# Performance work log

Hardware: AMD Instinct MI355X
Metric: run time of the kernel (lower is better)

The kernel has to match this reference:

```python
import jax, jax.numpy as jnp
import numpy as np

NUM_SEGMENTS = 64  # number of bags
L, D, F = 1024, 256, 32  # D = L/4, F = D/8, K = 1
EPS = 1e-12  # torch F.normalize eps


def setup_inputs() -> dict:
    key = jax.random.key(0)
    ks = jax.random.split(key, 10)
    N = 262144
    x = jax.random.normal(ks[0], (N, L), dtype=jnp.float32)
    idxs = jnp.sort(jax.random.randint(ks[1], (N,), 0, NUM_SEGMENTS)).astype(jnp.int64)
    sc = lambda fan_in: 1.0 / np.sqrt(fan_in)
    W1 = jax.random.uniform(ks[2], (L, D), jnp.float32, -sc(L), sc(L))
    b1 = jax.random.uniform(ks[3], (D,), jnp.float32, -sc(L), sc(L))
    Wa1 = jax.random.uniform(ks[4], (D, F), jnp.float32, -sc(D), sc(D))
    ba1 = jax.random.uniform(ks[5], (F,), jnp.float32, -sc(D), sc(D))
    Wa2 = jax.random.uniform(ks[6], (F, 1), jnp.float32, -sc(F), sc(F))
    ba2 = jax.random.uniform(ks[7], (1,), jnp.float32, -sc(F), sc(F))
    Wp = jax.random.uniform(ks[8], (D, F), jnp.float32, -sc(D), sc(D))
    bp = jax.random.uniform(ks[9], (F,), jnp.float32, -sc(D), sc(D))
    return {"x": x, "idxs": idxs, "W1": W1, "b1": b1, "Wa1": Wa1, "ba1": ba1,
            "Wa2": Wa2, "ba2": ba2, "Wp": Wp, "bp": bp}


def reference(x, idxs, W1, b1, Wa1, ba1, Wa2, ba2, Wp, bp):
    seg = idxs.astype(jnp.int32)
    # feature extractor (Dropout is identity in eval): H [N, D]
    H = x @ W1 + b1
    # attention logits: tanh MLP -> [N]
    logits = (jnp.tanh(H @ Wa1 + ba1) @ Wa2 + ba2)[:, 0]
    # segment softmax over instances within each bag
    m = jax.ops.segment_max(logits, seg, num_segments=NUM_SEGMENTS)
    e = jnp.exp(logits - m[seg])
    s = jax.ops.segment_sum(e, seg, num_segments=NUM_SEGMENTS)
    w = e / s[seg]  # [N]
    # attention-weighted bag embeddings: M [B, D]
    M = jax.ops.segment_sum(w[:, None] * H, seg, num_segments=NUM_SEGMENTS)
    # projector + L2 normalize (torch F.normalize: x / max(||x||, eps))
    proj = M @ Wp + bp
    norm = jnp.linalg.norm(proj, axis=1, keepdims=True)
    proj = proj / jnp.maximum(norm, EPS)
    return (M, proj)
```

## Files before the change

kernel.cpp:

```cpp
#include <hip/hip_runtime.h>
#include <stdint.h>

#define LDIM 1024
#define DDIM 256
#define FDIM 32
#define NSEG 64
#define BM 128
#define BK 64

typedef __attribute__((ext_vector_type(4))) float f32x4;
typedef __attribute__((ext_vector_type(8))) short short8;
typedef __attribute__((ext_vector_type(4))) unsigned int u32x4;

__device__ __forceinline__ unsigned int pk2bf(float a, float b) {
  union { float f; unsigned int u; } x, y; x.f = a; y.f = b;
  unsigned int ua = x.u + 0x7FFFu + ((x.u >> 16) & 1u);
  unsigned int ub = y.u + 0x7FFFu + ((y.u >> 16) & 1u);
  return (ua >> 16) | (ub & 0xFFFF0000u);
}

__device__ __forceinline__ unsigned short f2bf(float f) {
  union { float f; unsigned int u; } v; v.f = f;
  unsigned int r = v.u + 0x7FFFu + ((v.u >> 16) & 1u);
  return (unsigned short)(r >> 16);
}

__global__ void prep_w1t(const float* __restrict__ W1, const float* __restrict__ Wa1,
                         unsigned short* __restrict__ w1t) {
  __shared__ float rowf[DDIM];
  const int k = blockIdx.x;
  const int t = threadIdx.x;
  float v = W1[(size_t)k * DDIM + t];
  rowf[t] = v;
  w1t[(size_t)t * LDIM + k] = f2bf(v);
  __syncthreads();
  if (t < FDIM) {
    float a = 0.f;
    for (int c = 0; c < DDIM; ++c) a += rowf[c] * Wa1[c * FDIM + t];
    w1t[(size_t)(DDIM + t) * LDIM + k] = f2bf(a);
  }
}

__global__ void prep_misc(const float* __restrict__ b1, const float* __restrict__ Wa1,
                          const float* __restrict__ ba1, float* __restrict__ bz,
                          float* __restrict__ acc_eh, float* __restrict__ accE) {
  const int b = blockIdx.x, t = threadIdx.x;
  acc_eh[b * DDIM + t] = 0.f;
  if (t == 0) accE[b] = 0.f;
  if (b == 0 && t < FDIM) {
    float a = ba1[t];
    for (int c = 0; c < DDIM; ++c) a += b1[c] * Wa1[c * FDIM + t];
    bz[t] = a;
  }
}

__global__ __launch_bounds__(512) void fused_main(
    const float* __restrict__ x, const int* __restrict__ idxs,
    const unsigned short* __restrict__ w1t, const float* __restrict__ bz,
    const float* __restrict__ Wa2, const float* __restrict__ ba2,
    float* __restrict__ acc_eh, float* __restrict__ accE)
{
  __shared__ __align__(16) unsigned short xlds[BM][72];
  __shared__ __align__(16) unsigned char blds[320 * 128];
  __shared__ float logit_s[BM];
  __shared__ float e_s[BM];
  __shared__ int seg_s[BM];

  const int tid = threadIdx.x;
  const int lane = tid & 63;
  const int wid = tid >> 6;
  const int wr = wid >> 2;
  const int wc = wid & 3;
  const int g = lane >> 4;
  const int cl = lane & 15;
  const int row0 = blockIdx.x * BM;
  const int zf = (wc < 2) ? wc : -1;

  if (tid < BM) { seg_s[tid] = idxs[row0 + tid]; logit_s[tid] = 0.f; }

  f32x4 acc[4][4];
  f32x4 zacc[4];
  const f32x4 zero4 = {0.f, 0.f, 0.f, 0.f};
  #pragma unroll
  for (int m = 0; m < 4; ++m) {
    zacc[m] = zero4;
    #pragma unroll
    for (int n = 0; n < 4; ++n) acc[m][n] = zero4;
  }

  const int arow = tid >> 2;
  const int aq = tid & 3;
  const char* w1tb = (const char*)w1t;

  f32x4 ra[4], rb[4];
  {
    const float* gx = x + (size_t)(row0 + arow) * LDIM + aq * 16;
    ra[0] = *(const f32x4*)(gx);
    ra[1] = *(const f32x4*)(gx + 4);
    ra[2] = *(const f32x4*)(gx + 8);
    ra[3] = *(const f32x4*)(gx + 12);
  }

  auto do_iter = [&](int kt, f32x4 (&rc)[4], f32x4 (&rn)[4]) {
    __syncthreads();
    u32x4 p0, p1;
    p0[0] = pk2bf(rc[0][0], rc[0][1]); p0[1] = pk2bf(rc[0][2], rc[0][3]);
    p0[2] = pk2bf(rc[1][0], rc[1][1]); p0[3] = pk2bf(rc[1][2], rc[1][3]);
    p1[0] = pk2bf(rc[2][0], rc[2][1]); p1[1] = pk2bf(rc[2][2], rc[2][3]);
    p1[2] = pk2bf(rc[3][0], rc[3][1]); p1[3] = pk2bf(rc[3][2], rc[3][3]);
    *(u32x4*)&xlds[arow][aq * 16] = p0;
    *(u32x4*)&xlds[arow][aq * 16 + 8] = p1;
    #pragma unroll
    for (int j = 0; j < 5; ++j) {
      int idx = j * 512 + tid;
      int brow = idx >> 3;
      int bcolb = (idx & 7) << 4;
      int srcb = (brow << 11) + (kt << 7) + (bcolb ^ ((brow & 7) << 4));
      __builtin_amdgcn_global_load_lds(
          (const __attribute__((address_space(1))) unsigned int*)(w1tb + srcb),
          (__attribute__((address_space(3))) unsigned int*)(blds + j * 8192 + wid * 1024),
          16, 0, 0);
    }
    __syncthreads();
    if (kt < 15) {
      const float* gx = x + (size_t)(row0 + arow) * LDIM + (kt + 1) * BK + aq * 16;
      rn[0] = *(const f32x4*)(gx);
      rn[1] = *(const f32x4*)(gx + 4);
      rn[2] = *(const f32x4*)(gx + 8);
      rn[3] = *(const f32x4*)(gx + 12);
    }
    #pragma unroll
    for (int kk = 0; kk < 2; ++kk) {
      short8 af[4], bfr[4];
      #pragma unroll
      for (int m = 0; m < 4; ++m)
        af[m] = *(const short8*)((const char*)xlds + (wr * 64 + m * 16 + cl) * 144 + kk * 64 + g * 16);
      #pragma unroll
      for (int n = 0; n < 4; ++n) {
        int br = wc * 64 + n * 16 + cl;
        bfr[n] = *(const short8*)(blds + br * 128 + ((kk * 64 + g * 16) ^ ((br & 7) << 4)));
      }
      #pragma unroll
      for (int m = 0; m < 4; ++m)
        #pragma unroll
        for (int n = 0; n < 4; ++n)
          acc[m][n] = __builtin_amdgcn_mfma_f32_16x16x32_bf16(af[m], bfr[n], acc[m][n], 0, 0, 0);
      if (zf >= 0) {
        int br = DDIM + zf * 16 + cl;
        short8 zb = *(const short8*)(blds + br * 128 + ((kk * 64 + g * 16) ^ ((br & 7) << 4)));
        #pragma unroll
        for (int m = 0; m < 4; ++m)
          zacc[m] = __builtin_amdgcn_mfma_f32_16x16x32_bf16(af[m], zb, zacc[m], 0, 0, 0);
      }
    }
  };

  #pragma unroll 1
  for (int kt2 = 0; kt2 < 16; kt2 += 2) {
    do_iter(kt2, ra, rb);
    do_iter(kt2 + 1, rb, ra);
  }

  if (zf >= 0) {
    const int f = zf * 16 + cl;
    const float w2 = Wa2[f];
    const float bzf = bz[f];
    #pragma unroll
    for (int m = 0; m < 4; ++m) {
      float p[4];
      #pragma unroll
      for (int r = 0; r < 4; ++r) {
        float e2 = exp2f((zacc[m][r] + bzf) * 2.8853900817779268f);
        p[r] = (1.f - 2.f / (e2 + 1.f)) * w2;
      }
      #pragma unroll
      for (int mask = 1; mask <= 8; mask <<= 1)
        #pragma unroll
        for (int r = 0; r < 4; ++r)
          p[r] += __shfl_xor(p[r], mask);
      if (cl == 0) {
        #pragma unroll
        for (int r = 0; r < 4; ++r)
          atomicAdd(&logit_s[wr * 64 + m * 16 + g * 4 + r], p[r]);
      }
    }
  }
  __syncthreads();
  if (tid < BM) e_s[tid] = expf(logit_s[tid] + ba2[0]);
  __syncthreads();

  const int smin = seg_s[0];
  const int smax = seg_s[BM - 1];
  float ev[16]; int sv[16];
  #pragma unroll
  for (int m = 0; m < 4; ++m)
    #pragma unroll
    for (int r = 0; r < 4; ++r) {
      int rl = wr * 64 + m * 16 + g * 4 + r;
      ev[m * 4 + r] = e_s[rl];
      sv[m * 4 + r] = seg_s[rl];
    }
  for (int s = smin; s <= smax; ++s) {
    float wv[16];
    #pragma unroll
    for (int i = 0; i < 16; ++i) wv[i] = (sv[i] == s) ? ev[i] : 0.f;
    #pragma unroll
    for (int n = 0; n < 4; ++n) {
      float cs = 0.f;
      #pragma unroll
      for (int m = 0; m < 4; ++m)
        #pragma unroll
        for (int r = 0; r < 4; ++r)
          cs += wv[m * 4 + r] * acc[m][n][r];
      cs += __shfl_xor(cs, 16);
      cs += __shfl_xor(cs, 32);
      if (lane < 16) atomicAdd(&acc_eh[s * DDIM + wc * 64 + n * 16 + cl], cs);
    }
    if (wid < 2) {
      int rl = wid * 64 + lane;
      float v = (seg_s[rl] == s) ? e_s[rl] : 0.f;
      #pragma unroll
      for (int mask = 1; mask <= 32; mask <<= 1) v += __shfl_xor(v, mask);
      if (lane == 0) atomicAdd(&accE[s], v);
    }
  }
}

__global__ void finalize_k(const float* __restrict__ acc_eh, const float* __restrict__ accE,
                           const float* __restrict__ b1, const float* __restrict__ Wp,
                           const float* __restrict__ bp, float* __restrict__ out) {
  __shared__ float Ml[DDIM];
  const int s = blockIdx.x, t = threadIdx.x;
  const float E = accE[s];
  float m = 0.f;
  if (E > 0.f) m = acc_eh[s * DDIM + t] / E + b1[t];
  out[s * DDIM + t] = m;
  Ml[t] = m;
  __syncthreads();
  if (t < FDIM) {
    float p = bp[t];
    for (int c = 0; c < DDIM; ++c) p += Ml[c] * Wp[c * FDIM + t];
    float n2 = p * p;
    #pragma unroll
    for (int mask = 1; mask <= 16; mask <<= 1) n2 += __shfl_xor(n2, mask);
    out[NSEG * DDIM + s * FDIM + t] = p / fmaxf(sqrtf(n2), 1e-12f);
  }
}

extern "C" void kernel_launch(void* const* d_in, const int* in_sizes, int n_in,
                              void* d_out, int out_size, void* d_ws, size_t ws_size,
                              hipStream_t stream) {
  const float* x   = (const float*)d_in[0];
  const int*   idxs= (const int*)d_in[1];
  const float* W1  = (const float*)d_in[2];
  const float* b1  = (const float*)d_in[3];
  const float* Wa1 = (const float*)d_in[4];
  const float* ba1 = (const float*)d_in[5];
  const float* Wa2 = (const float*)d_in[6];
  const float* ba2 = (const float*)d_in[7];
  const float* Wp  = (const float*)d_in[8];
  const float* bp  = (const float*)d_in[9];
  float* out = (float*)d_out;

  char* ws = (char*)d_ws;
  unsigned short* w1t = (unsigned short*)ws;
  float* bz     = (float*)(ws + 655360);
  float* acc_eh = (float*)(ws + 655488);
  float* accE   = (float*)(ws + 721024);

  const int n = in_sizes[1];
  prep_w1t<<<LDIM, DDIM, 0, stream>>>(W1, Wa1, w1t);
  prep_misc<<<NSEG, DDIM, 0, stream>>>(b1, Wa1, ba1, bz, acc_eh, accE);
  fused_main<<<n / BM, 512, 0, stream>>>(x, idxs, w1t, bz, Wa2, ba2, acc_eh, accE);
  finalize_k<<<NSEG, DDIM, 0, stream>>>(acc_eh, accE, b1, Wp, bp, out);
}
```

Measured before the change: 352.1 us.

## Shrink row tile to 64 with 4 waves and drop logit padding

The fused GEMM tile shrinks from 128 to 64 rows, and the block drops from 8 to 4 waves with a launch bound asking for 3 blocks per CU. Each wave now computes a 32x144 slice covering 256 H columns plus 32 attention columns, so only 288 of 320 weight rows are staged and the old padded z-MFMA path is removed. The logit partials are written directly instead of via shared atomics, and the separate double-buffered register sets for x are merged into one. The aim is higher occupancy and less wasted MFMA work. The cost is that the staged weight tile is reused across half as many rows, doubling W1 traffic from L2 per row, and the kernel now issues twice as many blocks and per-segment atomics.

After: 1.050 ms. 198% more time.

```diff
diff --git a/kernel.cpp b/kernel.cpp
--- a/kernel.cpp
+++ b/kernel.cpp
@@ -5,8 +5,9 @@
 #define DDIM 256
 #define FDIM 32
 #define NSEG 64
-#define BM 128
+#define BM 64
 #define BK 64
+#define NWAVE 4
 
 typedef __attribute__((ext_vector_type(4))) float f32x4;
 typedef __attribute__((ext_vector_type(8))) short short8;
@@ -54,14 +55,14 @@
   }
 }
 
-__global__ __launch_bounds__(512) void fused_main(
+__global__ __launch_bounds__(256, 3) void fused_main(
     const float* __restrict__ x, const int* __restrict__ idxs,
     const unsigned short* __restrict__ w1t, const float* __restrict__ bz,
     const float* __restrict__ Wa2, const float* __restrict__ ba2,
     float* __restrict__ acc_eh, float* __restrict__ accE)
 {
   __shared__ __align__(16) unsigned short xlds[BM][72];
-  __shared__ __align__(16) unsigned char blds[320 * 128];
+  __shared__ __align__(16) unsigned char blds[288 * 128];
   __shared__ float logit_s[BM];
   __shared__ float e_s[BM];
   __shared__ int seg_s[BM];
@@ -69,119 +70,97 @@
   const int tid = threadIdx.x;
   const int lane = tid & 63;
   const int wid = tid >> 6;
-  const int wr = wid >> 2;
-  const int wc = wid & 3;
+  const int wr = wid >> 1;
+  const int wc = wid & 1;
   const int g = lane >> 4;
   const int cl = lane & 15;
   const int row0 = blockIdx.x * BM;
-  const int zf = (wc < 2) ? wc : -1;
-
-  if (tid < BM) { seg_s[tid] = idxs[row0 + tid]; logit_s[tid] = 0.f; }
-
-  f32x4 acc[4][4];
-  f32x4 zacc[4];
+
+  if (tid < BM) seg_s[tid] = idxs[row0 + tid];
+
+  f32x4 acc[2][9];
   const f32x4 zero4 = {0.f, 0.f, 0.f, 0.f};
   #pragma unroll
-  for (int m = 0; m < 4; ++m) {
-    zacc[m] = zero4;
-    #pragma unroll
-    for (int n = 0; n < 4; ++n) acc[m][n] = zero4;
-  }
+  for (int m = 0; m < 2; ++m)
+    #pragma unroll
+    for (int n = 0; n < 9; ++n) acc[m][n] = zero4;
 
   const int arow = tid >> 2;
   const int aq = tid & 3;
   const char* w1tb = (const char*)w1t;
 
-  f32x4 ra[4], rb[4];
+  f32x4 r0, r1, r2, r3;
   {
     const float* gx = x + (size_t)(row0 + arow) * LDIM + aq * 16;
-    ra[0] = *(const f32x4*)(gx);
-    ra[1] = *(const f32x4*)(gx + 4);
-    ra[2] = *(const f32x4*)(gx + 8);
-    ra[3] = *(const f32x4*)(gx + 12);
-  }
-
-  auto do_iter = [&](int kt, f32x4 (&rc)[4], f32x4 (&rn)[4]) {
+    r0 = *(const f32x4*)(gx);
+    r1 = *(const f32x4*)(gx + 4);
+    r2 = *(const f32x4*)(gx + 8);
+    r3 = *(const f32x4*)(gx + 12);
+  }
+
+  #pragma unroll 1
+  for (int kt = 0; kt < 16; ++kt) {
     __syncthreads();
+    #pragma unroll
+    for (int j = 0; j < 9; ++j) {
+      int byteoff = j * 4096 + tid * 16;
+      int brow = byteoff >> 7;
+      int bcolb = byteoff & 127;
+      int srcb = brow * 2048 + kt * 128 + (bcolb ^ ((brow & 7) << 4));
+      __builtin_amdgcn_global_load_lds(
+          (const __attribute__((address_space(1))) unsigned int*)(w1tb + srcb),
+          (__attribute__((address_space(3))) unsigned int*)(blds + j * 4096 + wid * 1024),
+          16, 0, 0);
+    }
     u32x4 p0, p1;
-    p0[0] = pk2bf(rc[0][0], rc[0][1]); p0[1] = pk2bf(rc[0][2], rc[0][3]);
-    p0[2] = pk2bf(rc[1][0], rc[1][1]); p0[3] = pk2bf(rc[1][2], rc[1][3]);
-    p1[0] = pk2bf(rc[2][0], rc[2][1]); p1[1] = pk2bf(rc[2][2], rc[2][3]);
-    p1[2] = pk2bf(rc[3][0], rc[3][1]); p1[3] = pk2bf(rc[3][2], rc[3][3]);
+    p0[0] = pk2bf(r0[0], r0[1]); p0[1] = pk2bf(r0[2], r0[3]);
+    p0[2] = pk2bf(r1[0], r1[1]); p0[3] = pk2bf(r1[2], r1[3]);
+    p1[0] = pk2bf(r2[0], r2[1]); p1[1] = pk2bf(r2[2], r2[3]);
+    p1[2] = pk2bf(r3[0], r3[1]); p1[3] = pk2bf(r3[2], r3[3]);
     *(u32x4*)&xlds[arow][aq * 16] = p0;
     *(u32x4*)&xlds[arow][aq * 16 + 8] = p1;
-    #pragma unroll
-    for (int j = 0; j < 5; ++j) {
-      int idx = j * 512 + tid;
-      int brow = idx >> 3;
-      int bcolb = (idx & 7) << 4;
-      int srcb = (brow << 11) + (kt << 7) + (bcolb ^ ((brow & 7) << 4));
-      __builtin_amdgcn_global_load_lds(
-          (const __attribute__((address_space(1))) unsigned int*)(w1tb + srcb),
-          (__attribute__((address_space(3))) unsigned int*)(blds + j * 8192 + wid * 1024),
-          16, 0, 0);
-    }
     __syncthreads();
     if (kt < 15) {
       const float* gx = x + (size_t)(row0 + arow) * LDIM + (kt + 1) * BK + aq * 16;
-      rn[0] = *(const f32x4*)(gx);
-      rn[1] = *(const f32x4*)(gx + 4);
-      rn[2] = *(const f32x4*)(gx + 8);
-      rn[3] = *(const f32x4*)(gx + 12);
+      r0 = *(const f32x4*)(gx);
+      r1 = *(const f32x4*)(gx + 4);
+      r2 = *(const f32x4*)(gx + 8);
+      r3 = *(const f32x4*)(gx + 12);
     }
     #pragma unroll
     for (int kk = 0; kk < 2; ++kk) {
-      short8 af[4], bfr[4];
-      #pragma unroll
-      for (int m = 0; m < 4; ++m)
-        af[m] = *(const short8*)((const char*)xlds + (wr * 64 + m * 16 + cl) * 144 + kk * 64 + g * 16);
-      #pragma unroll
-      for (int n = 0; n < 4; ++n) {
-        int br = wc * 64 + n * 16 + cl;
-        bfr[n] = *(const short8*)(blds + br * 128 + ((kk * 64 + g * 16) ^ ((br & 7) << 4)));
+      short8 af0 = *(const short8*)((const char*)xlds + (wr * 32 + cl) * 144 + kk * 64 + g * 16);
+      short8 af1 = *(const short8*)((const char*)xlds + (wr * 32 + 16 + cl) * 144 + kk * 64 + g * 16);
+      #pragma unroll
+      for (int n = 0; n < 9; ++n) {
+        int brr = wc * 144 + n * 16 + cl;
+        short8 bf = *(const short8*)(blds + brr * 128 + ((kk * 64 + g * 16) ^ ((brr & 7) << 4)));
+        acc[0][n] = __builtin_amdgcn_mfma_f32_16x16x32_bf16(af0, bf, acc[0][n], 0, 0, 0);
+        acc[1][n] = __builtin_amdgcn_mfma_f32_16x16x32_bf16(af1, bf, acc[1][n], 0, 0, 0);
       }
-      #pragma unroll
-      for (int m = 0; m < 4; ++m)
-        #pragma unroll
-        for (int n = 0; n < 4; ++n)
-          acc[m][n] = __builtin_amdgcn_mfma_f32_16x16x32_bf16(af[m], bfr[n], acc[m][n], 0, 0, 0);
-      if (zf >= 0) {
-        int br = DDIM + zf * 16 + cl;
-        short8 zb = *(const short8*)(blds + br * 128 + ((kk * 64 + g * 16) ^ ((br & 7) << 4)));
-        #pragma unroll
-        for (int m = 0; m < 4; ++m)
-          zacc[m] = __builtin_amdgcn_mfma_f32_16x16x32_bf16(af[m], zb, zacc[m], 0, 0, 0);
-      }
-    }
-  };
-
-  #pragma unroll 1
-  for (int kt2 = 0; kt2 < 16; kt2 += 2) {
-    do_iter(kt2, ra, rb);
-    do_iter(kt2 + 1, rb, ra);
-  }
-
-  if (zf >= 0) {
-    const int f = zf * 16 + cl;
-    const float w2 = Wa2[f];
-    const float bzf = bz[f];
-    #pragma unroll
-    for (int m = 0; m < 4; ++m) {
+    }
+  }
+
+  if (wc == 1) {
+    const float w2a = Wa2[cl], w2b = Wa2[16 + cl];
+    const float bza = bz[cl], bzb = bz[16 + cl];
+    #pragma unroll
+    for (int m = 0; m < 2; ++m) {
       float p[4];
       #pragma unroll
-      for (int r = 0; r < 4; ++r) {
-        float e2 = exp2f((zacc[m][r] + bzf) * 2.8853900817779268f);
-        p[r] = (1.f - 2.f / (e2 + 1.f)) * w2;
+      for (int q = 0; q < 4; ++q) {
+        float ea = exp2f((acc[m][7][q] + bza) * 2.8853900817779268f);
+        float eb = exp2f((acc[m][8][q] + bzb) * 2.8853900817779268f);
+        p[q] = (1.f - 2.f / (ea + 1.f)) * w2a + (1.f - 2.f / (eb + 1.f)) * w2b;
       }
       #pragma unroll
       for (int mask = 1; mask <= 8; mask <<= 1)
         #pragma unroll
-        for (int r = 0; r < 4; ++r)
-          p[r] += __shfl_xor(p[r], mask);
+        for (int q = 0; q < 4; ++q) p[q] += __shfl_xor(p[q], mask);
       if (cl == 0) {
         #pragma unroll
-        for (int r = 0; r < 4; ++r)
-          atomicAdd(&logit_s[wr * 64 + m * 16 + g * 4 + r], p[r]);
+        for (int q = 0; q < 4; ++q)
+          logit_s[wr * 32 + m * 16 + g * 4 + q] = p[q];
       }
     }
   }
@@ -191,34 +170,33 @@
 
   const int smin = seg_s[0];
   const int smax = seg_s[BM - 1];
-  float ev[16]; int sv[16];
+  float ev[8]; int sv[8];
   #pragma unroll
-  for (int m = 0; m < 4; ++m)
-    #pragma unroll
-    for (int r = 0; r < 4; ++r) {
-      int rl = wr * 64 + m * 16 + g * 4 + r;
-      ev[m * 4 + r] = e_s[rl];
-      sv[m * 4 + r] = seg_s[rl];
-    }
+  for (int m = 0; m < 2; ++m)
+    #pragma unroll
+    for (int q = 0; q < 4; ++q) {
+      int rl = wr * 32 + m * 16 + g * 4 + q;
+      ev[m * 4 + q] = e_s[rl];
+      sv[m * 4 + q] = seg_s[rl];
+    }
+  const int nmax = (wc == 0) ? 9 : 7;
   for (int s = smin; s <= smax; ++s) {
-    float wv[16];
-    #pragma unroll
-    for (int i = 0; i < 16; ++i) wv[i] = (sv[i] == s) ? ev[i] : 0.f;
-    #pragma unroll
-    for (int n = 0; n < 4; ++n) {
+    float wv[8];
+    #pragma unroll
+    for (int i = 0; i < 8; ++i) wv[i] = (sv[i] == s) ? ev[i] : 0.f;
+    for (int n = 0; n < nmax; ++n) {
       float cs = 0.f;
       #pragma unroll
-      for (int m = 0; m < 4; ++m)
+      for (int m = 0; m < 2; ++m)
         #pragma unroll
-        for (int r = 0; r < 4; ++r)
-          cs += wv[m * 4 + r] * acc[m][n][r];
+        for (int q = 0; q < 4; ++q)
+          cs += wv[m * 4 + q] * acc[m][n][q];
       cs += __shfl_xor(cs, 16);
       cs += __shfl_xor(cs, 32);
-      if (lane < 16) atomicAdd(&acc_eh[s * DDIM + wc * 64 + n * 16 + cl], cs);
-    }
-    if (wid < 2) {
-      int rl = wid * 64 + lane;
-      float v = (seg_s[rl] == s) ? e_s[rl] : 0.f;
+      if (lane < 16) atomicAdd(&acc_eh[s * DDIM + wc * 144 + n * 16 + cl], cs);
+    }
+    if (wid == 0) {
+      float v = (seg_s[lane] == s) ? e_s[lane] : 0.f;
       #pragma unroll
       for (int mask = 1; mask <= 32; mask <<= 1) v += __shfl_xor(v, mask);
       if (lane == 0) atomicAdd(&accE[s], v);
@@ -271,6 +249,6 @@
   const int n = in_sizes[1];
   prep_w1t<<<LDIM, DDIM, 0, stream>>>(W1, Wa1, w1t);
   prep_misc<<<NSEG, DDIM, 0, stream>>>(b1, Wa1, ba1, bz, acc_eh, accE);
-  fused_main<<<n / BM, 512, 0, stream>>>(x, idxs, w1t, bz, Wa2, ba2, acc_eh, accE);
+  fused_main<<<n / BM, 256, 0, stream>>>(x, idxs, w1t, bz, Wa2, ba2, acc_eh, accE);
   finalize_k<<<NSEG, DDIM, 0, stream>>>(acc_eh, accE, b1, Wp, bp, out);
 }
```
